# Kernel optimization log

Measured on AMD Instinct MI355X. Metric: run time of the kernel, lower is better.

## Reference

```python
import jax, jax.numpy as jnp
import numpy as np

N_NODES = 50000
N_EDGES = 625000
D = 128
H = 128

def setup_inputs() -> dict:
    key = jax.random.key(0)
    ks = jax.random.split(key, 6)
    z = jax.random.normal(ks[0], (N_NODES, D), dtype=jnp.float32)
    edge_index = jax.random.randint(ks[1], (2, N_EDGES), 0, N_NODES, dtype=jnp.int64)
    # MLP params (Linear stores y = x @ W + b here; W is [in, out])
    W1 = jax.random.normal(ks[2], (2 * D, H), dtype=jnp.float32) * (1.0 / np.sqrt(2 * D))
    b1 = jnp.zeros((H,), dtype=jnp.float32)
    W2 = jax.random.normal(ks[3], (H, H // 2), dtype=jnp.float32) * (1.0 / np.sqrt(H))
    b2 = jnp.zeros((H // 2,), dtype=jnp.float32)
    W3 = jax.random.normal(ks[4], (H // 2, 1), dtype=jnp.float32) * (1.0 / np.sqrt(H // 2))
    b3 = jnp.zeros((1,), dtype=jnp.float32)
    return {"z": z, "edge_index": edge_index, "W1": W1, "b1": b1,
            "W2": W2, "b2": b2, "W3": W3, "b3": b3}

def reference(z, edge_index, W1, b1, W2, b2, W3, b3):
    # Gather edge endpoints: z_i [E, D], z_j [E, D]
    z_i = z[edge_index[0]]
    z_j = z[edge_index[1]]
    edge_feat = jnp.concatenate([z_i, z_j], axis=-1)  # [E, 2D]
    h = jax.nn.relu(edge_feat @ W1 + b1)              # [E, H]  (dropout = identity, eval)
    h = jax.nn.relu(h @ W2 + b2)                      # [E, H//2]
    scores = (h @ W3 + b3)[:, 0]                      # [E]
    return scores
```

## Files before the change

### kernel.cpp

```cpp
#include <hip/hip_runtime.h>

#define NEDGE 625000
#define NNODE 50000
#define WPITCH 136
#define EPITCH 68
#define WCPITCH 136

typedef __bf16 bf16x8 __attribute__((ext_vector_type(8)));
typedef unsigned short u16x8 __attribute__((ext_vector_type(8)));
typedef float f32x4 __attribute__((ext_vector_type(4)));

__device__ __forceinline__ unsigned short f32_bf16(float f) {
  __bf16 h = (__bf16)f;
  return __builtin_bit_cast(unsigned short, h);
}
__device__ __forceinline__ float bf16_f32(unsigned short h) {
  return (float)__builtin_bit_cast(__bf16, h);
}

__global__ __launch_bounds__(256, 2) void uv_kernel(
    const float* __restrict__ z, const float* __restrict__ W1,
    const float* __restrict__ b1, const float* __restrict__ W2,
    const int* __restrict__ ei,
    unsigned short* __restrict__ UV, unsigned short* __restrict__ W2T,
    int* __restrict__ idx64_flag)
{
  __shared__ unsigned short lWc[256 * WCPITCH];
  __shared__ unsigned short st[4 * 16 * EPITCH];
  const int t = threadIdx.x, wave = t >> 6, lane = t & 63, c = lane & 15, q = lane >> 4;
  const int bid = blockIdx.x;

  if (bid < 2) {
    for (int e = bid * 4096 + t; e < (bid + 1) * 4096; e += 256) {
      int n = e >> 7, k = e & 127;
      W2T[n * 128 + k] = f32_bf16(W2[k * 64 + n]);
    }
  }
  if (bid == 0 && t == 0) {
    int allz = 1;
    for (int j = 1; j < 64; j += 2) allz &= (ei[j] == 0);
    *idx64_flag = allz;
  }

  for (int e = t; e < 256 * 128; e += 256) {
    int r = e >> 7, j = e & 127;
    float v = W1[r * 128 + j];
    int jp = (r < 128) ? j : (128 + j);
    int k = r & 127;
    lWc[jp * WCPITCH + k] = f32_bf16(v);
  }
  __syncthreads();

  const int mbase = bid * 64 + wave * 16;
  const int rA = mbase + c;
  const int rAc = (rA < NNODE) ? rA : 0;

  bf16x8 a0[4];
  {
    const float* zA = z + (size_t)rAc * 128 + q * 8;
    float4 fA[4][2];
#pragma unroll
    for (int kt = 0; kt < 4; ++kt) {
      fA[kt][0] = ((const float4*)(zA + kt * 32))[0];
      fA[kt][1] = ((const float4*)(zA + kt * 32))[1];
    }
#pragma unroll
    for (int kt = 0; kt < 4; ++kt) {
      const float* pa = (const float*)&fA[kt][0];
      bf16x8 oa;
#pragma unroll
      for (int j = 0; j < 8; ++j) oa[j] = (__bf16)pa[j];
      a0[kt] = oa;
    }
  }

  unsigned short* my = &st[wave * 16 * EPITCH];

  for (int nc = 0; nc < 4; ++nc) {
    f32x4 acc[4];
#pragma unroll
    for (int nt = 0; nt < 4; ++nt) {
      f32x4 zz = {0.f, 0.f, 0.f, 0.f};
      acc[nt] = zz;
    }
#pragma unroll
    for (int kt = 0; kt < 4; ++kt)
#pragma unroll
      for (int nt = 0; nt < 4; ++nt) {
        bf16x8 bb = *(const bf16x8*)(&lWc[(nc * 64 + nt * 16 + c) * WCPITCH + kt * 32 + q * 8]);
        acc[nt] = __builtin_amdgcn_mfma_f32_16x16x32_bf16(a0[kt], bb, acc[nt], 0, 0, 0);
      }

    float badd[4];
#pragma unroll
    for (int nt = 0; nt < 4; ++nt) {
      int col = nc * 64 + nt * 16 + c;
      badd[nt] = (col < 128) ? b1[col] : 0.f;
    }

#pragma unroll
    for (int nt = 0; nt < 4; ++nt)
#pragma unroll
      for (int reg = 0; reg < 4; ++reg)
        my[(q * 4 + reg) * EPITCH + nt * 16 + c] = f32_bf16(acc[nt][reg] + badd[nt]);
    __asm__ volatile("s_waitcnt lgkmcnt(0)" ::: "memory");

    {
      int lrow = lane >> 2, qt = lane & 3;
      int grow = mbase + lrow;
      u16x8 d0 = *(u16x8*)&my[lrow * EPITCH + qt * 16 + 0];
      u16x8 d1 = *(u16x8*)&my[lrow * EPITCH + qt * 16 + 8];
      if (grow < NNODE) {
        u16x8* dst = (u16x8*)(UV + (size_t)grow * 256 + nc * 64 + qt * 16);
        dst[0] = d0;
        dst[1] = d1;
      }
    }
    __asm__ volatile("s_waitcnt lgkmcnt(0)" ::: "memory");
  }
}

__global__ __launch_bounds__(256, 4) void edge_kernel(
    const int* __restrict__ ei,
    const unsigned short* __restrict__ UV,
    const unsigned short* __restrict__ W2T,
    const float* __restrict__ b2, const float* __restrict__ W3,
    const float* __restrict__ b3, const int* __restrict__ idx64_flag,
    float* __restrict__ out)
{
  __shared__ unsigned short lW[64 * WPITCH];
  const int t = threadIdx.x, wave = t >> 6, lane = t & 63, c = lane & 15, q = lane >> 4;

  {
    int n = t >> 2, qd = t & 3;
    const u16x8* src = (const u16x8*)(W2T + n * 128 + qd * 32);
    u16x8* dst = (u16x8*)(&lW[n * WPITCH + qd * 32]);
#pragma unroll
    for (int i = 0; i < 4; ++i) dst[i] = src[i];
  }
  __syncthreads();

  const int ebase = blockIdx.x * 128 + wave * 32;
  const int eA = ebase + c, eB = ebase + 16 + c;
  const int eAc = (eA < NEDGE) ? eA : 0;
  const int eBc = (eB < NEDGE) ? eB : 0;
  int sA, dA, sB, dB;
  if (*idx64_flag) {
    const long long* e64 = (const long long*)ei;
    sA = (int)e64[eAc]; dA = (int)e64[NEDGE + eAc];
    sB = (int)e64[eBc]; dB = (int)e64[NEDGE + eBc];
  } else {
    sA = ei[eAc]; dA = ei[NEDGE + eAc];
    sB = ei[eBc]; dB = ei[NEDGE + eBc];
  }

  const u16x8* pAu = (const u16x8*)(UV + (size_t)sA * 256) + q;
  const u16x8* pAv = (const u16x8*)(UV + (size_t)dA * 256 + 128) + q;
  const u16x8* pBu = (const u16x8*)(UV + (size_t)sB * 256) + q;
  const u16x8* pBv = (const u16x8*)(UV + (size_t)dB * 256 + 128) + q;
  u16x8 rAu[4], rAv[4], rBu[4], rBv[4];
#pragma unroll
  for (int kt = 0; kt < 4; ++kt) {
    rAu[kt] = pAu[kt * 4];
    rAv[kt] = pAv[kt * 4];
    rBu[kt] = pBu[kt * 4];
    rBv[kt] = pBv[kt * 4];
  }

  f32x4 acc[2][4];
#pragma unroll
  for (int mt = 0; mt < 2; ++mt)
#pragma unroll
    for (int nt = 0; nt < 4; ++nt) {
      f32x4 zz = {0.f, 0.f, 0.f, 0.f};
      acc[mt][nt] = zz;
    }

#pragma unroll
  for (int kt = 0; kt < 4; ++kt) {
    bf16x8 a0, a1;
#pragma unroll
    for (int j = 0; j < 8; ++j) {
      a0[j] = (__bf16)fmaxf(bf16_f32(rAu[kt][j]) + bf16_f32(rAv[kt][j]), 0.f);
      a1[j] = (__bf16)fmaxf(bf16_f32(rBu[kt][j]) + bf16_f32(rBv[kt][j]), 0.f);
    }
#pragma unroll
    for (int nt = 0; nt < 4; ++nt) {
      bf16x8 bb = *(const bf16x8*)(&lW[(nt * 16 + c) * WPITCH + kt * 32 + q * 8]);
      acc[0][nt] = __builtin_amdgcn_mfma_f32_16x16x32_bf16(a0, bb, acc[0][nt], 0, 0, 0);
      acc[1][nt] = __builtin_amdgcn_mfma_f32_16x16x32_bf16(a1, bb, acc[1][nt], 0, 0, 0);
    }
  }

  float b2v[4], w3v[4];
#pragma unroll
  for (int nt = 0; nt < 4; ++nt) {
    int n = nt * 16 + c;
    b2v[nt] = b2[n];
    w3v[nt] = W3[n];
  }
  float bias3 = b3[0];

#pragma unroll
  for (int mt = 0; mt < 2; ++mt) {
    float p0 = 0.f, p1 = 0.f, p2 = 0.f, p3 = 0.f;
#pragma unroll
    for (int nt = 0; nt < 4; ++nt) {
      p0 += fmaxf(acc[mt][nt][0] + b2v[nt], 0.f) * w3v[nt];
      p1 += fmaxf(acc[mt][nt][1] + b2v[nt], 0.f) * w3v[nt];
      p2 += fmaxf(acc[mt][nt][2] + b2v[nt], 0.f) * w3v[nt];
      p3 += fmaxf(acc[mt][nt][3] + b2v[nt], 0.f) * w3v[nt];
    }
#pragma unroll
    for (int m = 1; m < 16; m <<= 1) {
      p0 += __shfl_xor(p0, m, 64);
      p1 += __shfl_xor(p1, m, 64);
      p2 += __shfl_xor(p2, m, 64);
      p3 += __shfl_xor(p3, m, 64);
    }
    if (c == 0) {
      int eb = ebase + mt * 16 + q * 4;
      if (eb + 0 < NEDGE) out[eb + 0] = p0 + bias3;
      if (eb + 1 < NEDGE) out[eb + 1] = p1 + bias3;
      if (eb + 2 < NEDGE) out[eb + 2] = p2 + bias3;
      if (eb + 3 < NEDGE) out[eb + 3] = p3 + bias3;
    }
  }
}

extern "C" void kernel_launch(void* const* d_in, const int* in_sizes, int n_in,
                              void* d_out, int out_size, void* d_ws, size_t ws_size,
                              hipStream_t stream) {
  const float* z  = (const float*)d_in[0];
  const int*   ei = (const int*)d_in[1];
  const float* W1 = (const float*)d_in[2];
  const float* b1 = (const float*)d_in[3];
  const float* W2 = (const float*)d_in[4];
  const float* b2 = (const float*)d_in[5];
  const float* W3 = (const float*)d_in[6];
  const float* b3 = (const float*)d_in[7];
  float* out = (float*)d_out;

  unsigned short* UV  = (unsigned short*)d_ws;
  unsigned short* W2T = UV + (size_t)NNODE * 256;
  int* idx64_flag     = (int*)(W2T + 64 * 128);

  uv_kernel<<<dim3((NNODE + 63) / 64), dim3(256), 0, stream>>>(
      z, W1, b1, W2, ei, UV, W2T, idx64_flag);
  edge_kernel<<<dim3((NEDGE + 127) / 128), dim3(256), 0, stream>>>(
      ei, UV, W2T, b2, W3, b3, idx64_flag, out);
}
```

Baseline: 152.5 us.

## Bucket edges by source node before the edge MLP to improve gather locality

Adds a sort pass that uses atomic counters to bin edges into fixed-capacity buckets of 128 source nodes, with an overflow region. A new edge kernel then processes each bucket tile and scatters scores back to the original edge ids. The aim is to make source-row UV gathers hit in cache more often. In exchange it adds a kernel launch, heavily contended atomics, extra index traffic and scattered output writes, and edges are silently dropped if the overflow region fills. The path is used only when the workspace is large enough.

```diff
diff --git a/kernel.cpp b/kernel.cpp
--- a/kernel.cpp
+++ b/kernel.cpp
@@ -6,6 +6,11 @@
 #define EPITCH 68
 #define WCPITCH 136
 
+#define NBUCK 391
+#define BCAP 2048
+#define OVCAP 4096
+#define BSTRIDE 16
+
 typedef __bf16 bf16x8 __attribute__((ext_vector_type(8)));
 typedef unsigned short u16x8 __attribute__((ext_vector_type(8)));
 typedef float f32x4 __attribute__((ext_vector_type(4)));
@@ -23,7 +28,7 @@
     const float* __restrict__ b1, const float* __restrict__ W2,
     const int* __restrict__ ei,
     unsigned short* __restrict__ UV, unsigned short* __restrict__ W2T,
-    int* __restrict__ idx64_flag)
+    int* __restrict__ idx64_flag, int* __restrict__ bins)
 {
   __shared__ unsigned short lWc[256 * WCPITCH];
   __shared__ unsigned short st[4 * 16 * EPITCH];
@@ -40,6 +45,9 @@
     int allz = 1;
     for (int j = 1; j < 64; j += 2) allz &= (ei[j] == 0);
     *idx64_flag = allz;
+  }
+  if (bid == 2 && bins != nullptr) {
+    for (int i = t; i < NBUCK * BSTRIDE + BSTRIDE; i += 256) bins[i] = 0;
   }
 
   for (int e = t; e < 256 * 128; e += 256) {
@@ -117,6 +125,164 @@
       }
     }
     __asm__ volatile("s_waitcnt lgkmcnt(0)" ::: "memory");
+  }
+}
+
+__global__ __launch_bounds__(256) void sort_kernel(
+    const int* __restrict__ ei, int* __restrict__ bins,
+    int* __restrict__ sSrc, int* __restrict__ sDst, int* __restrict__ sId)
+{
+  __shared__ int sflag;
+  const int t = threadIdx.x;
+  if (t < 64) {
+    int v = ei[t];
+    unsigned long long odd_nz = __ballot((t & 1) && v != 0);
+    if (t == 0) sflag = (odd_nz == 0ull) ? 1 : 0;
+  }
+  __syncthreads();
+  int e = blockIdx.x * 256 + t;
+  if (e >= NEDGE) return;
+  int src, dst;
+  if (sflag) {
+    const long long* e64 = (const long long*)ei;
+    src = (int)e64[e];
+    dst = (int)e64[NEDGE + e];
+  } else {
+    src = ei[e];
+    dst = ei[NEDGE + e];
+  }
+  int b = src >> 7;
+  int pos = atomicAdd(&bins[b * BSTRIDE], 1);
+  int slot;
+  if (pos < BCAP) {
+    slot = b * BCAP + pos;
+  } else {
+    int op = atomicAdd(&bins[NBUCK * BSTRIDE], 1);
+    if (op >= OVCAP) return;
+    slot = NBUCK * BCAP + op;
+  }
+  sSrc[slot] = src;
+  sDst[slot] = dst;
+  sId[slot] = e;
+}
+
+__global__ __launch_bounds__(256, 4) void edge_kernel_sorted(
+    const int* __restrict__ bins,
+    const int* __restrict__ sSrc, const int* __restrict__ sDst,
+    const int* __restrict__ sId,
+    const unsigned short* __restrict__ UV,
+    const unsigned short* __restrict__ W2T,
+    const float* __restrict__ b2, const float* __restrict__ W3,
+    const float* __restrict__ b3, float* __restrict__ out)
+{
+  __shared__ unsigned short lW[64 * WPITCH];
+  const int t = threadIdx.x, wave = t >> 6, lane = t & 63, c = lane & 15, q = lane >> 4;
+
+  {
+    int n = t >> 2, qd = t & 3;
+    const u16x8* src = (const u16x8*)(W2T + n * 128 + qd * 32);
+    u16x8* dst = (u16x8*)(&lW[n * WPITCH + qd * 32]);
+#pragma unroll
+    for (int i = 0; i < 4; ++i) dst[i] = src[i];
+  }
+  __syncthreads();
+
+  const int b = blockIdx.x;
+  int base, navail;
+  if (b < NBUCK * (BCAP / 128)) {
+    int bucket = b >> 4, tile = b & 15;
+    int cnt = bins[bucket * BSTRIDE];
+    if (cnt > BCAP) cnt = BCAP;
+    navail = cnt - tile * 128;
+    base = bucket * BCAP + tile * 128;
+  } else {
+    int tile = b - NBUCK * (BCAP / 128);
+    int cnt = bins[NBUCK * BSTRIDE];
+    if (cnt > OVCAP) cnt = OVCAP;
+    navail = cnt - tile * 128;
+    base = NBUCK * BCAP + tile * 128;
+  }
+  if (navail <= 0) return;
+  if (navail > 128) navail = 128;
+  if (wave * 32 >= navail) return;
+
+  const int liA = wave * 32 + c, liB = wave * 32 + 16 + c;
+  const int liAc = (liA < navail) ? liA : 0;
+  const int liBc = (liB < navail) ? liB : 0;
+  const int sA = sSrc[base + liAc], dA = sDst[base + liAc];
+  const int sB = sSrc[base + liBc], dB = sDst[base + liBc];
+
+  const u16x8* pAu = (const u16x8*)(UV + (size_t)sA * 256) + q;
+  const u16x8* pAv = (const u16x8*)(UV + (size_t)dA * 256 + 128) + q;
+  const u16x8* pBu = (const u16x8*)(UV + (size_t)sB * 256) + q;
+  const u16x8* pBv = (const u16x8*)(UV + (size_t)dB * 256 + 128) + q;
+  u16x8 rAu[4], rAv[4], rBu[4], rBv[4];
+#pragma unroll
+  for (int kt = 0; kt < 4; ++kt) {
+    rAu[kt] = pAu[kt * 4];
+    rAv[kt] = pAv[kt * 4];
+    rBu[kt] = pBu[kt * 4];
+    rBv[kt] = pBv[kt * 4];
+  }
+
+  f32x4 acc[2][4];
+#pragma unroll
+  for (int mt = 0; mt < 2; ++mt)
+#pragma unroll
+    for (int nt = 0; nt < 4; ++nt) {
+      f32x4 zz = {0.f, 0.f, 0.f, 0.f};
+      acc[mt][nt] = zz;
+    }
+
+#pragma unroll
+  for (int kt = 0; kt < 4; ++kt) {
+    bf16x8 a0, a1;
+#pragma unroll
+    for (int j = 0; j < 8; ++j) {
+      a0[j] = (__bf16)fmaxf(bf16_f32(rAu[kt][j]) + bf16_f32(rAv[kt][j]), 0.f);
+      a1[j] = (__bf16)fmaxf(bf16_f32(rBu[kt][j]) + bf16_f32(rBv[kt][j]), 0.f);
+    }
+#pragma unroll
+    for (int nt = 0; nt < 4; ++nt) {
+      bf16x8 bb = *(const bf16x8*)(&lW[(nt * 16 + c) * WPITCH + kt * 32 + q * 8]);
+      acc[0][nt] = __builtin_amdgcn_mfma_f32_16x16x32_bf16(a0, bb, acc[0][nt], 0, 0, 0);
+      acc[1][nt] = __builtin_amdgcn_mfma_f32_16x16x32_bf16(a1, bb, acc[1][nt], 0, 0, 0);
+    }
+  }
+
+  float b2v[4], w3v[4];
+#pragma unroll
+  for (int nt = 0; nt < 4; ++nt) {
+    int n = nt * 16 + c;
+    b2v[nt] = b2[n];
+    w3v[nt] = W3[n];
+  }
+  float bias3 = b3[0];
+
+#pragma unroll
+  for (int mt = 0; mt < 2; ++mt) {
+    float p0 = 0.f, p1 = 0.f, p2 = 0.f, p3 = 0.f;
+#pragma unroll
+    for (int nt = 0; nt < 4; ++nt) {
+      p0 += fmaxf(acc[mt][nt][0] + b2v[nt], 0.f) * w3v[nt];
+      p1 += fmaxf(acc[mt][nt][1] + b2v[nt], 0.f) * w3v[nt];
+      p2 += fmaxf(acc[mt][nt][2] + b2v[nt], 0.f) * w3v[nt];
+      p3 += fmaxf(acc[mt][nt][3] + b2v[nt], 0.f) * w3v[nt];
+    }
+#pragma unroll
+    for (int m = 1; m < 16; m <<= 1) {
+      p0 += __shfl_xor(p0, m, 64);
+      p1 += __shfl_xor(p1, m, 64);
+      p2 += __shfl_xor(p2, m, 64);
+      p3 += __shfl_xor(p3, m, 64);
+    }
+    if (c == 0) {
+      int lb = wave * 32 + mt * 16 + q * 4;
+      if (lb + 0 < navail) out[sId[base + lb + 0]] = p0 + bias3;
+      if (lb + 1 < navail) out[sId[base + lb + 1]] = p1 + bias3;
+      if (lb + 2 < navail) out[sId[base + lb + 2]] = p2 + bias3;
+      if (lb + 3 < navail) out[sId[base + lb + 3]] = p3 + bias3;
+    }
   }
 }
 
@@ -241,12 +407,27 @@
   const float* b3 = (const float*)d_in[7];
   float* out = (float*)d_out;
 
-  unsigned short* UV  = (unsigned short*)d_ws;
-  unsigned short* W2T = UV + (size_t)NNODE * 256;
-  int* idx64_flag     = (int*)(W2T + 64 * 128);
+  char* ws = (char*)d_ws;
+  size_t off = 0;
+  unsigned short* UV = (unsigned short*)(ws + off); off += (size_t)NNODE * 256 * 2;
+  unsigned short* W2T = (unsigned short*)(ws + off); off += 64 * 128 * 2;
+  int* idx64_flag = (int*)(ws + off); off += 16;
+  int* bins = (int*)(ws + off); off += (size_t)(NBUCK * BSTRIDE + BSTRIDE) * 4;
+  const size_t nslot = (size_t)NBUCK * BCAP + OVCAP;
+  int* sSrc = (int*)(ws + off); off += nslot * 4;
+  int* sDst = (int*)(ws + off); off += nslot * 4;
+  int* sId  = (int*)(ws + off); off += nslot * 4;
+  const bool do_sort = (ws_size >= off);
 
   uv_kernel<<<dim3((NNODE + 63) / 64), dim3(256), 0, stream>>>(
-      z, W1, b1, W2, ei, UV, W2T, idx64_flag);
-  edge_kernel<<<dim3((NEDGE + 127) / 128), dim3(256), 0, stream>>>(
-      ei, UV, W2T, b2, W3, b3, idx64_flag, out);
-}
+      z, W1, b1, W2, ei, UV, W2T, idx64_flag, do_sort ? bins : nullptr);
+  if (do_sort) {
+    sort_kernel<<<dim3((NEDGE + 255) / 256), dim3(256), 0, stream>>>(
+        ei, bins, sSrc, sDst, sId);
+    edge_kernel_sorted<<<dim3(NBUCK * (BCAP / 128) + OVCAP / 128), dim3(256), 0, stream>>>(
+        bins, sSrc, sDst, sId, UV, W2T, b2, W3, b3, out);
+  } else {
+    edge_kernel<<<dim3((NEDGE + 127) / 128), dim3(256), 0, stream>>>(
+        ei, UV, W2T, b2, W3, b3, idx64_flag, out);
+  }
+}
```

Measured after the change: 210.6 us. +38.1%, slower.
